# Kernel tuning notes

Hardware: AMD Instinct MI355X
Metric: run time of the kernel (lower is better)

The kernel has to match this reference:

```python
import jax, jax.numpy as jnp
import numpy as np

N_USERS = 100_000
N_ITEMS = 100_000
D = 64
B = 16_384
L_U = 50   # items per user history
N_F = 32   # friends per user
L_I = 50   # users per item history


def setup_inputs() -> dict:
    key = jax.random.key(0)
    ks = jax.random.split(key, 22)
    s = 0.1  # xavier-ish scale for D=64
    return {
        "user_ids": jax.random.randint(ks[0], (B,), 0, N_USERS),
        "item_ids": jax.random.randint(ks[1], (B,), 0, N_ITEMS),
        "user_hist_items": jax.random.randint(ks[2], (B, L_U), 0, N_ITEMS),
        "user_hist_ratings": jax.random.uniform(ks[3], (B, L_U), jnp.float32, 1.0, 5.0),
        "user_friends": jax.random.randint(ks[4], (B, N_F), 0, N_USERS),
        "item_hist_users": jax.random.randint(ks[5], (B, L_I), 0, N_USERS),
        "item_hist_ratings": jax.random.uniform(ks[6], (B, L_I), jnp.float32, 1.0, 5.0),
        "embed_user": jax.random.normal(ks[7], (N_USERS, D), jnp.float32) * s,
        "embed_item": jax.random.normal(ks[8], (N_ITEMS, D), jnp.float32) * s,
        "W1": jax.random.normal(ks[9], (D, D), jnp.float32) * s,
        "W2": jax.random.normal(ks[10], (D, D), jnp.float32) * s,
        "W3": jax.random.normal(ks[11], (D, 1), jnp.float32) * s,
        "W4": jax.random.normal(ks[12], (D, D), jnp.float32) * s,
        "W5": jax.random.normal(ks[13], (D, D), jnp.float32) * s,
        "W6": jax.random.normal(ks[14], (D, 1), jnp.float32) * s,
        "W7": jax.random.normal(ks[15], (D, D), jnp.float32) * s,
        "W8": jax.random.normal(ks[16], (D, D), jnp.float32) * s,
        "W9": jax.random.normal(ks[17], (D, 1), jnp.float32) * s,
        "fc1_w": jax.random.normal(ks[18], (2 * D, D), jnp.float32) * s,
        "fc1_b": jnp.zeros((D,), jnp.float32),
        "fc2_w": jax.random.normal(ks[19], (D, 1), jnp.float32) * s,
        "fc2_b": jnp.zeros((1,), jnp.float32),
    }


def _attention(q_emb, neigh, Wq, Wk, Wa, ratings=None):
    # q_emb: [B, D]; neigh: [B, L, D]; ratings: [B, L] or None
    a = q_emb @ Wq  # [B, D]
    a = a[:, None, :] + neigh @ Wk  # [B, L, D]
    if ratings is not None:
        a = a + ratings[..., None] * neigh
    w = jax.nn.softmax((a @ Wa)[..., 0], axis=1)  # [B, L]
    return jnp.einsum("bl,bld->bd", w, neigh)


def reference(user_ids, item_ids, user_hist_items, user_hist_ratings,
              user_friends, item_hist_users, item_hist_ratings,
              embed_user, embed_item,
              W1, W2, W3, W4, W5, W6, W7, W8, W9,
              fc1_w, fc1_b, fc2_w, fc2_b):
    user_emb = embed_user[user_ids]          # [B, D]
    item_emb = embed_item[item_ids]          # [B, D]

    # user <- rated items attention (W1, W2, W3)
    hist_item_embs = embed_item[user_hist_items]        # [B, L_U, D]
    user_items_emb = _attention(user_emb, hist_item_embs, W1, W2, W3,
                                user_hist_ratings)

    # user <- friends attention (W4, W5, W6)
    friend_embs = embed_user[user_friends]               # [B, N_F, D]
    user_social_emb = _attention(user_emb, friend_embs, W4, W5, W6)

    user_emb_final = user_emb + user_items_emb + user_social_emb

    # item <- interacting users attention (W7, W8, W9)
    hist_user_embs = embed_user[item_hist_users]         # [B, L_I, D]
    item_users_emb = _attention(item_emb, hist_user_embs, W7, W8, W9,
                                item_hist_ratings)
    item_emb_final = item_emb + item_users_emb

    concat = jnp.concatenate([user_emb_final, item_emb_final], axis=1)  # [B, 2D]
    h = jax.nn.relu(concat @ fc1_w + fc1_b)
    out = (h @ fc2_w + fc2_b)[:, 0]  # [B]
    return out
```

## Files before the change

kernel.cpp:

```cpp
#include <hip/hip_runtime.h>
#include <math.h>

#define B_TOTAL 16384
#define D 64
#define L_U 50
#define N_F 32
#define L_I 50

#define WAVE_FL 512

__global__ void graphrec_setup(const float* __restrict__ W2, const float* __restrict__ W3,
                               const float* __restrict__ W5, const float* __restrict__ W6,
                               const float* __restrict__ W8, const float* __restrict__ W9,
                               float* __restrict__ u) {
    int t = threadIdx.x;
    int w = t >> 6;
    int d = t & 63;
    const float* Wm;
    const float* Wv;
    int off;
    switch (w) {
        case 0: Wm = W2; Wv = W3; off = 64;  break;
        case 1: Wm = W5; Wv = W6; off = 192; break;
        default: Wm = W8; Wv = W9; off = 320; break;
    }
    float s = 0.f;
    #pragma unroll
    for (int j = 0; j < D; ++j) s = fmaf(Wm[d * D + j], Wv[j], s);
    u[off + d] = s;
}

__device__ __forceinline__ float wred_sum(float x) {
    float t;
    #define STEP_ADD(ctrl, rmask)                                                        \
        t = __int_as_float(__builtin_amdgcn_update_dpp(0, __float_as_int(x),             \
                                                       ctrl, rmask, 0xf, false));        \
        x = x + t;
    STEP_ADD(0x111, 0xf)
    STEP_ADD(0x112, 0xf)
    STEP_ADD(0x114, 0xf)
    STEP_ADD(0x118, 0xf)
    STEP_ADD(0x142, 0xa)
    STEP_ADD(0x143, 0xc)
    #undef STEP_ADD
    return __int_as_float(__builtin_amdgcn_readlane(__float_as_int(x), 63));
}

__device__ __forceinline__ float segred8(float x) {
    float t;
    t = __int_as_float(__builtin_amdgcn_update_dpp(0, __float_as_int(x), 0x111, 0xf, 0xf, false));
    x = x + t;
    t = __int_as_float(__builtin_amdgcn_update_dpp(0, __float_as_int(x), 0x112, 0xf, 0xf, false));
    x = x + t;
    t = __int_as_float(__builtin_amdgcn_update_dpp(0, __float_as_int(x), 0x114, 0xf, 0xf, false));
    x = x + t;
    return x;
}

__device__ __forceinline__ float dot8(float4 n0, float4 n1, float4 u0, float4 u1) {
    return fmaf(n0.x, u0.x, fmaf(n0.y, u0.y, fmaf(n0.z, u0.z, fmaf(n0.w, u0.w,
           fmaf(n1.x, u1.x, fmaf(n1.y, u1.y, fmaf(n1.z, u1.z, n1.w * u1.w)))))));
}

template <int L, int NG, bool HAS_R>
__device__ __forceinline__ float attn_online(const float* __restrict__ u2,
                                             const float* __restrict__ wa, float rv,
                                             int lane, int sub, int cc, int co,
                                             const float* __restrict__ table, int idxreg,
                                             float* __restrict__ part) {
    const float4 uu0 = ((const float4*)u2)[2 * cc];
    const float4 uu1 = ((const float4*)u2)[2 * cc + 1];
    float4 ww0 = {0.f, 0.f, 0.f, 0.f}, ww1 = {0.f, 0.f, 0.f, 0.f};
    if (HAS_R) {
        ww0 = ((const float4*)wa)[2 * cc];
        ww1 = ((const float4*)wa)[2 * cc + 1];
    }

    float4 st0[2], st1[2];
    float srr[2] = {0.f, 0.f};
    #pragma unroll
    for (int p = 0; p < 2; ++p) {
        const int slot = 8 * p + sub;
        const int rid = __builtin_amdgcn_ds_bpermute(slot << 2, idxreg);
        if (HAS_R)
            srr[p] = __int_as_float(
                __builtin_amdgcn_ds_bpermute(slot << 2, __float_as_int(rv)));
        const float* pp = table + (unsigned)((rid << 6) + co);
        st0[p] = ((const float4*)pp)[0];
        st1[p] = ((const float4*)pp)[1];
    }

    float sum = 0.f;
    float4 a0 = {0.f, 0.f, 0.f, 0.f}, a1 = {0.f, 0.f, 0.f, 0.f};
    #pragma unroll
    for (int g = 0; g < NG; ++g) {
        const int pi = g & 1;
        const float4 n0 = st0[pi];
        const float4 n1 = st1[pi];
        const float rrow = srr[pi];
        if (g + 2 < NG) {
            const int slot2 = 8 * (g + 2) + sub;
            const int sl2 = (slot2 > L - 1) ? (L - 1) : slot2;
            const int rid2 = __builtin_amdgcn_ds_bpermute(sl2 << 2, idxreg);
            if (HAS_R)
                srr[pi] = __int_as_float(
                    __builtin_amdgcn_ds_bpermute(sl2 << 2, __float_as_int(rv)));
            const float* pp2 = table + (unsigned)((rid2 << 6) + co);
            st0[pi] = ((const float4*)pp2)[0];
            st1[pi] = ((const float4*)pp2)[1];
        }
        float4 c0, c1;
        if (HAS_R) {
            c0.x = fmaf(rrow, ww0.x, uu0.x); c0.y = fmaf(rrow, ww0.y, uu0.y);
            c0.z = fmaf(rrow, ww0.z, uu0.z); c0.w = fmaf(rrow, ww0.w, uu0.w);
            c1.x = fmaf(rrow, ww1.x, uu1.x); c1.y = fmaf(rrow, ww1.y, uu1.y);
            c1.z = fmaf(rrow, ww1.z, uu1.z); c1.w = fmaf(rrow, ww1.w, uu1.w);
        } else {
            c0 = uu0; c1 = uu1;
        }
        const float pd = segred8(dot8(n0, n1, c0, c1));
        float e = __expf(__int_as_float(
            __builtin_amdgcn_ds_swizzle(__float_as_int(pd), 0xF8)));
        if (8 * g + sub >= L) e = 0.f;
        sum += e;
        a0.x = fmaf(e, n0.x, a0.x); a0.y = fmaf(e, n0.y, a0.y);
        a0.z = fmaf(e, n0.z, a0.z); a0.w = fmaf(e, n0.w, a0.w);
        a1.x = fmaf(e, n1.x, a1.x); a1.y = fmaf(e, n1.y, a1.y);
        a1.z = fmaf(e, n1.z, a1.z); a1.w = fmaf(e, n1.w, a1.w);
    }

    const float S = wred_sum((cc == 7) ? sum : 0.f);

    const int s4 = lane & 4;
    const int pw = lane << 3;
    *(float4*)(part + pw + s4)       = a0;
    *(float4*)(part + pw + (4 ^ s4)) = a1;
    const int rb = (lane & 56) + ((lane & 7) ^ ((lane >> 3) & 4));
    float acc = 0.f;
    #pragma unroll
    for (int s2 = 0; s2 < 8; ++s2) acc += part[rb + 64 * s2];
    return acc * (1.0f / S);
}

__global__ __launch_bounds__(256) void graphrec_fwd(
        const int* __restrict__ user_ids, const int* __restrict__ item_ids,
        const int* __restrict__ uh_items, const float* __restrict__ uh_rat,
        const int* __restrict__ ufriends,
        const int* __restrict__ ih_users, const float* __restrict__ ih_rat,
        const float* __restrict__ eu, const float* __restrict__ ei,
        const float* __restrict__ W3, const float* __restrict__ W6,
        const float* __restrict__ W9,
        const float* __restrict__ fc1w, const float* __restrict__ fc1b,
        const float* __restrict__ fc2w, const float* __restrict__ fc2b,
        const float* __restrict__ u, float* __restrict__ out) {
    __shared__ __align__(16) float smem[4 * WAVE_FL];
    const int lane = threadIdx.x & 63;
    const int wv = threadIdx.x >> 6;
    const int b = blockIdx.x * 4 + wv;
    float* part = smem + wv * WAVE_FL;
    const int sub = lane >> 3;
    const int cc  = lane & 7;
    const int co  = cc << 3;

    int idxA = 0, idxB = 0, idxC = 0;
    float rA = 0.f, rC = 0.f;
    if (lane < L_U) {
        idxA = uh_items[b * L_U + lane];
        rA   = uh_rat[b * L_U + lane];
        idxC = ih_users[b * L_I + lane];
        rC   = ih_rat[b * L_I + lane];
    }
    if (lane < N_F) idxB = ufriends[b * N_F + lane];

    const int uid = user_ids[b];
    const int iid = item_ids[b];
    const float qu = eu[(size_t)uid * D + lane];
    const float qi = ei[(size_t)iid * D + lane];

    const float accA = attn_online<L_U, 7, true >(u + 64, W3, rA,
                                                  lane, sub, cc, co, ei, idxA, part);
    const float accB = attn_online<N_F, 4, false>(u + 192, W6, 0.f,
                                                  lane, sub, cc, co, eu, idxB, part);
    const float accC = attn_online<L_I, 7, true >(u + 320, W9, rC,
                                                  lane, sub, cc, co, eu, idxC, part);

    const float uf  = qu + accA + accB;
    const float itf = qi + accC;

    float h0 = fc1b[lane], h1 = 0.f, h2 = 0.f, h3 = 0.f;
    #pragma unroll
    for (int k = 0; k < D; k += 4) {
        h0 = fmaf(__int_as_float(__builtin_amdgcn_readlane(__float_as_int(uf), k + 0)),
                  fc1w[(k + 0) * D + lane], h0);
        h1 = fmaf(__int_as_float(__builtin_amdgcn_readlane(__float_as_int(uf), k + 1)),
                  fc1w[(k + 1) * D + lane], h1);
        h2 = fmaf(__int_as_float(__builtin_amdgcn_readlane(__float_as_int(uf), k + 2)),
                  fc1w[(k + 2) * D + lane], h2);
        h3 = fmaf(__int_as_float(__builtin_amdgcn_readlane(__float_as_int(uf), k + 3)),
                  fc1w[(k + 3) * D + lane], h3);
    }
    #pragma unroll
    for (int k = 0; k < D; k += 4) {
        h0 = fmaf(__int_as_float(__builtin_amdgcn_readlane(__float_as_int(itf), k + 0)),
                  fc1w[(D + k + 0) * D + lane], h0);
        h1 = fmaf(__int_as_float(__builtin_amdgcn_readlane(__float_as_int(itf), k + 1)),
                  fc1w[(D + k + 1) * D + lane], h1);
        h2 = fmaf(__int_as_float(__builtin_amdgcn_readlane(__float_as_int(itf), k + 2)),
                  fc1w[(D + k + 2) * D + lane], h2);
        h3 = fmaf(__int_as_float(__builtin_amdgcn_readlane(__float_as_int(itf), k + 3)),
                  fc1w[(D + k + 3) * D + lane], h3);
    }
    const float h = fmaxf((h0 + h1) + (h2 + h3), 0.f);
    const float o = wred_sum(h * fc2w[lane]);
    if (lane == 0) out[b] = o + fc2b[0];
}

extern "C" void kernel_launch(void* const* d_in, const int* in_sizes, int n_in,
                              void* d_out, int out_size, void* d_ws, size_t ws_size,
                              hipStream_t stream) {
    const int*   user_ids = (const int*)d_in[0];
    const int*   item_ids = (const int*)d_in[1];
    const int*   uh_items = (const int*)d_in[2];
    const float* uh_rat   = (const float*)d_in[3];
    const int*   ufriends = (const int*)d_in[4];
    const int*   ih_users = (const int*)d_in[5];
    const float* ih_rat   = (const float*)d_in[6];
    const float* eu       = (const float*)d_in[7];
    const float* ei       = (const float*)d_in[8];
    const float* W3 = (const float*)d_in[11];
    const float* W6 = (const float*)d_in[14];
    const float* W9 = (const float*)d_in[17];
    const float* W2 = (const float*)d_in[10];
    const float* W5 = (const float*)d_in[13];
    const float* W8 = (const float*)d_in[16];
    const float* fc1w = (const float*)d_in[18];
    const float* fc1b = (const float*)d_in[19];
    const float* fc2w = (const float*)d_in[20];
    const float* fc2b = (const float*)d_in[21];
    float* out = (float*)d_out;
    float* u   = (float*)d_ws;

    graphrec_setup<<<1, 192, 0, stream>>>(W2, W3, W5, W6, W8, W9, u);
    graphrec_fwd<<<B_TOTAL / 4, 256, 0, stream>>>(
        user_ids, item_ids, uh_items, uh_rat, ufriends, ih_users, ih_rat,
        eu, ei, W3, W6, W9, fc1w, fc1b, fc2w, fc2b, u, out);
}
```

Measured before the change: 200.8 us.

## Stream neighbor rows via async global-to-LDS ring with deep cross-phase prefetch

Replaces the register double-buffered gathers with direct global_load_lds copies into a 7-slot per-wave LDS ring. One continuous stream of 34 groups spans all three attention phases, kept 6 groups ahead with explicit vmcnt waits, so later phases' gathers overlap earlier compute. Each lane now covers 4 columns with 4 rows per group instead of 8 columns and 8 rows, and the coefficient vectors are staged once in shared memory. In exchange it needs more LDS per block, hand-counted waitcnt values that must match the issue order, and more loop iterations with longer reductions.

```diff
diff --git a/kernel.cpp b/kernel.cpp
--- a/kernel.cpp
+++ b/kernel.cpp
@@ -7,7 +7,21 @@
 #define N_F 32
 #define L_I 50
 
-#define WAVE_FL 512
+#define NG_A 13
+#define NG_B 8
+#define NG_C 13
+#define NSTREAM 34
+#define NSLOT 7
+#define SLOT_FL 256
+#define RING_FL (NSLOT * SLOT_FL)
+#define FOLD_FL 256
+#define WAVE_FL (RING_FL + FOLD_FL)
+#define COEF_FL 320
+
+#define WAITV(n) asm volatile("s_waitcnt vmcnt(" #n ")" ::: "memory")
+
+typedef unsigned int u32_g __attribute__((address_space(1)));
+typedef unsigned int u32_l __attribute__((address_space(3)));
 
 __global__ void graphrec_setup(const float* __restrict__ W2, const float* __restrict__ W3,
                                const float* __restrict__ W5, const float* __restrict__ W6,
@@ -46,7 +60,7 @@
     return __int_as_float(__builtin_amdgcn_readlane(__float_as_int(x), 63));
 }
 
-__device__ __forceinline__ float segred8(float x) {
+__device__ __forceinline__ float segred16(float x) {
     float t;
     t = __int_as_float(__builtin_amdgcn_update_dpp(0, __float_as_int(x), 0x111, 0xf, 0xf, false));
     x = x + t;
@@ -54,91 +68,77 @@
     x = x + t;
     t = __int_as_float(__builtin_amdgcn_update_dpp(0, __float_as_int(x), 0x114, 0xf, 0xf, false));
     x = x + t;
+    t = __int_as_float(__builtin_amdgcn_update_dpp(0, __float_as_int(x), 0x118, 0xf, 0xf, false));
+    x = x + t;
     return x;
 }
 
-__device__ __forceinline__ float dot8(float4 n0, float4 n1, float4 u0, float4 u1) {
-    return fmaf(n0.x, u0.x, fmaf(n0.y, u0.y, fmaf(n0.z, u0.z, fmaf(n0.w, u0.w,
-           fmaf(n1.x, u1.x, fmaf(n1.y, u1.y, fmaf(n1.z, u1.z, n1.w * u1.w)))))));
-}
-
-template <int L, int NG, bool HAS_R>
-__device__ __forceinline__ float attn_online(const float* __restrict__ u2,
-                                             const float* __restrict__ wa, float rv,
-                                             int lane, int sub, int cc, int co,
-                                             const float* __restrict__ table, int idxreg,
-                                             float* __restrict__ part) {
-    const float4 uu0 = ((const float4*)u2)[2 * cc];
-    const float4 uu1 = ((const float4*)u2)[2 * cc + 1];
-    float4 ww0 = {0.f, 0.f, 0.f, 0.f}, ww1 = {0.f, 0.f, 0.f, 0.f};
-    if (HAS_R) {
-        ww0 = ((const float4*)wa)[2 * cc];
-        ww1 = ((const float4*)wa)[2 * cc + 1];
-    }
-
-    float4 st0[2], st1[2];
-    float srr[2] = {0.f, 0.f};
-    #pragma unroll
-    for (int p = 0; p < 2; ++p) {
-        const int slot = 8 * p + sub;
-        const int rid = __builtin_amdgcn_ds_bpermute(slot << 2, idxreg);
-        if (HAS_R)
-            srr[p] = __int_as_float(
-                __builtin_amdgcn_ds_bpermute(slot << 2, __float_as_int(rv)));
-        const float* pp = table + (unsigned)((rid << 6) + co);
-        st0[p] = ((const float4*)pp)[0];
-        st1[p] = ((const float4*)pp)[1];
-    }
+__device__ __forceinline__ void issue_group(int j, int sub, int cl,
+                                            const float* __restrict__ eu,
+                                            const float* __restrict__ ei,
+                                            int idxA, int idxB, int idxC,
+                                            float* ring) {
+    const float* table;
+    int idx, slot, L;
+    if (j < NG_A)               { table = ei; idx = idxA; slot = 4 * j + sub;            L = L_U; }
+    else if (j < NG_A + NG_B)   { table = eu; idx = idxB; slot = 4 * (j - NG_A) + sub;   L = N_F; }
+    else                        { table = eu; idx = idxC; slot = 4 * (j - NG_A - NG_B) + sub; L = L_I; }
+    if (slot > L - 1) slot = L - 1;
+    const int rid = __builtin_amdgcn_ds_bpermute(slot << 2, idx);
+    const float* g = table + (unsigned)((rid << 6) + (cl << 2));
+    float* dst = ring + (j % NSLOT) * SLOT_FL;
+    __builtin_amdgcn_global_load_lds((const u32_g*)g, (u32_l*)dst, 16, 0, 0);
+}
+
+template <int JBASE, int NG, int L, bool HAS_R>
+__device__ __forceinline__ float phase_run(const float* __restrict__ cf_u2,
+                                           const float* __restrict__ cf_wa,
+                                           float rv, int lane, int sub, int cl,
+                                           const float* __restrict__ eu,
+                                           const float* __restrict__ ei,
+                                           int idxA, int idxB, int idxC,
+                                           float* ring, float* fold) {
+    const float4 uu = *(const float4*)(cf_u2 + (cl << 2));
+    float4 ww = {0.f, 0.f, 0.f, 0.f};
+    if (HAS_R) ww = *(const float4*)(cf_wa + (cl << 2));
 
     float sum = 0.f;
-    float4 a0 = {0.f, 0.f, 0.f, 0.f}, a1 = {0.f, 0.f, 0.f, 0.f};
+    float4 a = {0.f, 0.f, 0.f, 0.f};
     #pragma unroll
     for (int g = 0; g < NG; ++g) {
-        const int pi = g & 1;
-        const float4 n0 = st0[pi];
-        const float4 n1 = st1[pi];
-        const float rrow = srr[pi];
-        if (g + 2 < NG) {
-            const int slot2 = 8 * (g + 2) + sub;
-            const int sl2 = (slot2 > L - 1) ? (L - 1) : slot2;
-            const int rid2 = __builtin_amdgcn_ds_bpermute(sl2 << 2, idxreg);
-            if (HAS_R)
-                srr[pi] = __int_as_float(
-                    __builtin_amdgcn_ds_bpermute(sl2 << 2, __float_as_int(rv)));
-            const float* pp2 = table + (unsigned)((rid2 << 6) + co);
-            st0[pi] = ((const float4*)pp2)[0];
-            st1[pi] = ((const float4*)pp2)[1];
+        const int J = JBASE + g;
+        if (J <= 28)      WAITV(5);
+        else if (J == 29) WAITV(4);
+        else if (J == 30) WAITV(3);
+        else if (J == 31) WAITV(2);
+        else if (J == 32) WAITV(1);
+        else              WAITV(0);
+        if (J + 6 < NSTREAM)
+            issue_group(J + 6, sub, cl, eu, ei, idxA, idxB, idxC, ring);
+        const float4 n = *(const float4*)(ring + (J % NSLOT) * SLOT_FL + (lane << 2));
+        float4 c = uu;
+        if (HAS_R) {
+            const int slot = 4 * g + sub;
+            const int sl = (slot > L - 1) ? (L - 1) : slot;
+            const float rrow = __int_as_float(
+                __builtin_amdgcn_ds_bpermute(sl << 2, __float_as_int(rv)));
+            c.x = fmaf(rrow, ww.x, uu.x); c.y = fmaf(rrow, ww.y, uu.y);
+            c.z = fmaf(rrow, ww.z, uu.z); c.w = fmaf(rrow, ww.w, uu.w);
         }
-        float4 c0, c1;
-        if (HAS_R) {
-            c0.x = fmaf(rrow, ww0.x, uu0.x); c0.y = fmaf(rrow, ww0.y, uu0.y);
-            c0.z = fmaf(rrow, ww0.z, uu0.z); c0.w = fmaf(rrow, ww0.w, uu0.w);
-            c1.x = fmaf(rrow, ww1.x, uu1.x); c1.y = fmaf(rrow, ww1.y, uu1.y);
-            c1.z = fmaf(rrow, ww1.z, uu1.z); c1.w = fmaf(rrow, ww1.w, uu1.w);
-        } else {
-            c0 = uu0; c1 = uu1;
-        }
-        const float pd = segred8(dot8(n0, n1, c0, c1));
+        float pd = fmaf(n.x, c.x, fmaf(n.y, c.y, fmaf(n.z, c.z, n.w * c.w)));
+        pd = segred16(pd);
         float e = __expf(__int_as_float(
-            __builtin_amdgcn_ds_swizzle(__float_as_int(pd), 0xF8)));
-        if (8 * g + sub >= L) e = 0.f;
+            __builtin_amdgcn_ds_swizzle(__float_as_int(pd), 0x1FF)));
+        if (4 * g + sub >= L) e = 0.f;
         sum += e;
-        a0.x = fmaf(e, n0.x, a0.x); a0.y = fmaf(e, n0.y, a0.y);
-        a0.z = fmaf(e, n0.z, a0.z); a0.w = fmaf(e, n0.w, a0.w);
-        a1.x = fmaf(e, n1.x, a1.x); a1.y = fmaf(e, n1.y, a1.y);
-        a1.z = fmaf(e, n1.z, a1.z); a1.w = fmaf(e, n1.w, a1.w);
-    }
-
-    const float S = wred_sum((cc == 7) ? sum : 0.f);
-
-    const int s4 = lane & 4;
-    const int pw = lane << 3;
-    *(float4*)(part + pw + s4)       = a0;
-    *(float4*)(part + pw + (4 ^ s4)) = a1;
-    const int rb = (lane & 56) + ((lane & 7) ^ ((lane >> 3) & 4));
-    float acc = 0.f;
-    #pragma unroll
-    for (int s2 = 0; s2 < 8; ++s2) acc += part[rb + 64 * s2];
+        a.x = fmaf(e, n.x, a.x); a.y = fmaf(e, n.y, a.y);
+        a.z = fmaf(e, n.z, a.z); a.w = fmaf(e, n.w, a.w);
+    }
+
+    const float S = wred_sum(((lane & 15) == 15) ? sum : 0.f);
+
+    *(float4*)(fold + (lane << 2)) = a;
+    const float acc = fold[lane] + fold[64 + lane] + fold[128 + lane] + fold[192 + lane];
     return acc * (1.0f / S);
 }
 
@@ -153,14 +153,28 @@
         const float* __restrict__ fc1w, const float* __restrict__ fc1b,
         const float* __restrict__ fc2w, const float* __restrict__ fc2b,
         const float* __restrict__ u, float* __restrict__ out) {
-    __shared__ __align__(16) float smem[4 * WAVE_FL];
+    __shared__ __align__(16) float smem[4 * WAVE_FL + COEF_FL];
     const int lane = threadIdx.x & 63;
     const int wv = threadIdx.x >> 6;
     const int b = blockIdx.x * 4 + wv;
-    float* part = smem + wv * WAVE_FL;
-    const int sub = lane >> 3;
-    const int cc  = lane & 7;
-    const int co  = cc << 3;
+    float* ring = smem + wv * WAVE_FL;
+    float* fold = ring + RING_FL;
+    float* cf   = smem + 4 * WAVE_FL;
+    const int sub = lane >> 4;
+    const int cl  = lane & 15;
+
+    for (int k = threadIdx.x; k < COEF_FL; k += 256) {
+        const int v = k >> 6, d = k & 63;
+        float val;
+        switch (v) {
+            case 0: val = u[64 + d];  break;
+            case 1: val = W3[d];      break;
+            case 2: val = u[192 + d]; break;
+            case 3: val = u[320 + d]; break;
+            default: val = W9[d];     break;
+        }
+        cf[k] = val;
+    }
 
     int idxA = 0, idxB = 0, idxC = 0;
     float rA = 0.f, rC = 0.f;
@@ -177,12 +191,18 @@
     const float qu = eu[(size_t)uid * D + lane];
     const float qi = ei[(size_t)iid * D + lane];
 
-    const float accA = attn_online<L_U, 7, true >(u + 64, W3, rA,
-                                                  lane, sub, cc, co, ei, idxA, part);
-    const float accB = attn_online<N_F, 4, false>(u + 192, W6, 0.f,
-                                                  lane, sub, cc, co, eu, idxB, part);
-    const float accC = attn_online<L_I, 7, true >(u + 320, W9, rC,
-                                                  lane, sub, cc, co, eu, idxC, part);
+    __syncthreads();
+
+    #pragma unroll
+    for (int j = 0; j < 6; ++j)
+        issue_group(j, sub, cl, eu, ei, idxA, idxB, idxC, ring);
+
+    const float accA = phase_run<0,          NG_A, L_U, true >(cf,       cf + 64, rA,
+                            lane, sub, cl, eu, ei, idxA, idxB, idxC, ring, fold);
+    const float accB = phase_run<NG_A,       NG_B, N_F, false>(cf + 128, cf,      0.f,
+                            lane, sub, cl, eu, ei, idxA, idxB, idxC, ring, fold);
+    const float accC = phase_run<NG_A + NG_B, NG_C, L_I, true >(cf + 192, cf + 256, rC,
+                            lane, sub, cl, eu, ei, idxA, idxB, idxC, ring, fold);
 
     const float uf  = qu + accA + accB;
     const float itf = qi + accC;
@@ -227,12 +247,12 @@
     const float* ih_rat   = (const float*)d_in[6];
     const float* eu       = (const float*)d_in[7];
     const float* ei       = (const float*)d_in[8];
+    const float* W2 = (const float*)d_in[10];
     const float* W3 = (const float*)d_in[11];
+    const float* W5 = (const float*)d_in[13];
     const float* W6 = (const float*)d_in[14];
+    const float* W8 = (const float*)d_in[16];
     const float* W9 = (const float*)d_in[17];
-    const float* W2 = (const float*)d_in[10];
-    const float* W5 = (const float*)d_in[13];
-    const float* W8 = (const float*)d_in[16];
     const float* fc1w = (const float*)d_in[18];
     const float* fc1b = (const float*)d_in[19];
     const float* fc2w = (const float*)d_in[20];
```

Result: no change. 198.8 us (-1.0%).

## Gather neighbor embeddings from fp16 copies of the tables converted each call

Applied to the files above, without the earlier changes.

Adds a kernel that converts both full embedding tables (100k x 64 each) to fp16 in the workspace on every call. The attention gathers then read half-width rows and widen them to fp32. The explicit two-deep register prefetch pipeline is replaced with a plain per-group load under a bounds guard. This aims to halve gather traffic, but converting the tables costs about 51 MB read and 25 MB written per call, which likely outweighs the savings on roughly 2.15M random row gathers. It also lowers precision of the neighbor embeddings.

```diff
diff --git a/kernel.cpp b/kernel.cpp
--- a/kernel.cpp
+++ b/kernel.cpp
@@ -1,4 +1,5 @@
 #include <hip/hip_runtime.h>
+#include <hip/hip_fp16.h>
 #include <math.h>
 
 #define B_TOTAL 16384
@@ -6,6 +7,8 @@
 #define L_U 50
 #define N_F 32
 #define L_I 50
+#define N_ROWS 100000
+#define TAB_ELEMS (N_ROWS * D)
 
 #define WAVE_FL 512
 
@@ -30,6 +33,23 @@
     u[off + d] = s;
 }
 
+__global__ void convert_tables(const float* __restrict__ eu, const float* __restrict__ ei,
+                               __half* __restrict__ euh, __half* __restrict__ eih) {
+    const int n4 = TAB_ELEMS / 4;
+    for (int i = blockIdx.x * 256 + threadIdx.x; i < 2 * n4; i += 2048 * 256) {
+        const bool first = (i < n4);
+        const int j = first ? i : i - n4;
+        const float4 v = first ? ((const float4*)eu)[j] : ((const float4*)ei)[j];
+        const __half2 h0 = __float22half2_rn(make_float2(v.x, v.y));
+        const __half2 h1 = __float22half2_rn(make_float2(v.z, v.w));
+        uint2 pk;
+        pk.x = *(const unsigned int*)&h0;
+        pk.y = *(const unsigned int*)&h1;
+        if (first) ((uint2*)euh)[j] = pk;
+        else       ((uint2*)eih)[j] = pk;
+    }
+}
+
 __device__ __forceinline__ float wred_sum(float x) {
     float t;
     #define STEP_ADD(ctrl, rmask)                                                        \
@@ -62,11 +82,11 @@
            fmaf(n1.x, u1.x, fmaf(n1.y, u1.y, fmaf(n1.z, u1.z, n1.w * u1.w)))))));
 }
 
-template <int L, int NG, bool HAS_R>
+template <int L, int NG, bool HAS_R, typename T>
 __device__ __forceinline__ float attn_online(const float* __restrict__ u2,
                                              const float* __restrict__ wa, float rv,
-                                             int lane, int sub, int cc, int co,
-                                             const float* __restrict__ table, int idxreg,
+                                             int lane, int sub, int cc,
+                                             const T* __restrict__ table, int idxreg,
                                              float* __restrict__ part) {
     const float4 uu0 = ((const float4*)u2)[2 * cc];
     const float4 uu1 = ((const float4*)u2)[2 * cc + 1];
@@ -76,57 +96,48 @@
         ww1 = ((const float4*)wa)[2 * cc + 1];
     }
 
-    float4 st0[2], st1[2];
-    float srr[2] = {0.f, 0.f};
-    #pragma unroll
-    for (int p = 0; p < 2; ++p) {
-        const int slot = 8 * p + sub;
-        const int rid = __builtin_amdgcn_ds_bpermute(slot << 2, idxreg);
-        if (HAS_R)
-            srr[p] = __int_as_float(
-                __builtin_amdgcn_ds_bpermute(slot << 2, __float_as_int(rv)));
-        const float* pp = table + (unsigned)((rid << 6) + co);
-        st0[p] = ((const float4*)pp)[0];
-        st1[p] = ((const float4*)pp)[1];
-    }
-
     float sum = 0.f;
     float4 a0 = {0.f, 0.f, 0.f, 0.f}, a1 = {0.f, 0.f, 0.f, 0.f};
     #pragma unroll
     for (int g = 0; g < NG; ++g) {
-        const int pi = g & 1;
-        const float4 n0 = st0[pi];
-        const float4 n1 = st1[pi];
-        const float rrow = srr[pi];
-        if (g + 2 < NG) {
-            const int slot2 = 8 * (g + 2) + sub;
-            const int sl2 = (slot2 > L - 1) ? (L - 1) : slot2;
-            const int rid2 = __builtin_amdgcn_ds_bpermute(sl2 << 2, idxreg);
-            if (HAS_R)
-                srr[pi] = __int_as_float(
-                    __builtin_amdgcn_ds_bpermute(sl2 << 2, __float_as_int(rv)));
-            const float* pp2 = table + (unsigned)((rid2 << 6) + co);
-            st0[pi] = ((const float4*)pp2)[0];
-            st1[pi] = ((const float4*)pp2)[1];
+        const int slot = 8 * g + sub;
+        const int rowid = __builtin_amdgcn_ds_bpermute(slot << 2, idxreg);
+        float rrow = 0.f;
+        if (HAS_R)
+            rrow = __int_as_float(
+                __builtin_amdgcn_ds_bpermute(slot << 2, __float_as_int(rv)));
+        if (slot < L) {
+            float4 n0, n1;
+            const T* p = table + (unsigned)((rowid << 6) + (cc << 3));
+            if constexpr (sizeof(T) == 2) {
+                const int4 raw = *(const int4*)p;
+                float2 f;
+                f = __half22float2(*(const __half2*)&raw.x); n0.x = f.x; n0.y = f.y;
+                f = __half22float2(*(const __half2*)&raw.y); n0.z = f.x; n0.w = f.y;
+                f = __half22float2(*(const __half2*)&raw.z); n1.x = f.x; n1.y = f.y;
+                f = __half22float2(*(const __half2*)&raw.w); n1.z = f.x; n1.w = f.y;
+            } else {
+                n0 = ((const float4*)p)[0];
+                n1 = ((const float4*)p)[1];
+            }
+            float4 c0, c1;
+            if (HAS_R) {
+                c0.x = fmaf(rrow, ww0.x, uu0.x); c0.y = fmaf(rrow, ww0.y, uu0.y);
+                c0.z = fmaf(rrow, ww0.z, uu0.z); c0.w = fmaf(rrow, ww0.w, uu0.w);
+                c1.x = fmaf(rrow, ww1.x, uu1.x); c1.y = fmaf(rrow, ww1.y, uu1.y);
+                c1.z = fmaf(rrow, ww1.z, uu1.z); c1.w = fmaf(rrow, ww1.w, uu1.w);
+            } else {
+                c0 = uu0; c1 = uu1;
+            }
+            const float pd = segred8(dot8(n0, n1, c0, c1));
+            const float e = __expf(__int_as_float(
+                __builtin_amdgcn_ds_swizzle(__float_as_int(pd), 0xF8)));
+            sum += e;
+            a0.x = fmaf(e, n0.x, a0.x); a0.y = fmaf(e, n0.y, a0.y);
+            a0.z = fmaf(e, n0.z, a0.z); a0.w = fmaf(e, n0.w, a0.w);
+            a1.x = fmaf(e, n1.x, a1.x); a1.y = fmaf(e, n1.y, a1.y);
+            a1.z = fmaf(e, n1.z, a1.z); a1.w = fmaf(e, n1.w, a1.w);
         }
-        float4 c0, c1;
-        if (HAS_R) {
-            c0.x = fmaf(rrow, ww0.x, uu0.x); c0.y = fmaf(rrow, ww0.y, uu0.y);
-            c0.z = fmaf(rrow, ww0.z, uu0.z); c0.w = fmaf(rrow, ww0.w, uu0.w);
-            c1.x = fmaf(rrow, ww1.x, uu1.x); c1.y = fmaf(rrow, ww1.y, uu1.y);
-            c1.z = fmaf(rrow, ww1.z, uu1.z); c1.w = fmaf(rrow, ww1.w, uu1.w);
-        } else {
-            c0 = uu0; c1 = uu1;
-        }
-        const float pd = segred8(dot8(n0, n1, c0, c1));
-        float e = __expf(__int_as_float(
-            __builtin_amdgcn_ds_swizzle(__float_as_int(pd), 0xF8)));
-        if (8 * g + sub >= L) e = 0.f;
-        sum += e;
-        a0.x = fmaf(e, n0.x, a0.x); a0.y = fmaf(e, n0.y, a0.y);
-        a0.z = fmaf(e, n0.z, a0.z); a0.w = fmaf(e, n0.w, a0.w);
-        a1.x = fmaf(e, n1.x, a1.x); a1.y = fmaf(e, n1.y, a1.y);
-        a1.z = fmaf(e, n1.z, a1.z); a1.w = fmaf(e, n1.w, a1.w);
     }
 
     const float S = wred_sum((cc == 7) ? sum : 0.f);
@@ -142,14 +153,15 @@
     return acc * (1.0f / S);
 }
 
+template <typename T>
 __global__ __launch_bounds__(256) void graphrec_fwd(
         const int* __restrict__ user_ids, const int* __restrict__ item_ids,
         const int* __restrict__ uh_items, const float* __restrict__ uh_rat,
         const int* __restrict__ ufriends,
         const int* __restrict__ ih_users, const float* __restrict__ ih_rat,
         const float* __restrict__ eu, const float* __restrict__ ei,
-        const float* __restrict__ W3, const float* __restrict__ W6,
-        const float* __restrict__ W9,
+        const T* __restrict__ tabU, const T* __restrict__ tabI,
+        const float* __restrict__ W3, const float* __restrict__ W9,
         const float* __restrict__ fc1w, const float* __restrict__ fc1b,
         const float* __restrict__ fc2w, const float* __restrict__ fc2b,
         const float* __restrict__ u, float* __restrict__ out) {
@@ -160,7 +172,6 @@
     float* part = smem + wv * WAVE_FL;
     const int sub = lane >> 3;
     const int cc  = lane & 7;
-    const int co  = cc << 3;
 
     int idxA = 0, idxB = 0, idxC = 0;
     float rA = 0.f, rC = 0.f;
@@ -177,12 +188,12 @@
     const float qu = eu[(size_t)uid * D + lane];
     const float qi = ei[(size_t)iid * D + lane];
 
-    const float accA = attn_online<L_U, 7, true >(u + 64, W3, rA,
-                                                  lane, sub, cc, co, ei, idxA, part);
-    const float accB = attn_online<N_F, 4, false>(u + 192, W6, 0.f,
-                                                  lane, sub, cc, co, eu, idxB, part);
-    const float accC = attn_online<L_I, 7, true >(u + 320, W9, rC,
-                                                  lane, sub, cc, co, eu, idxC, part);
+    const float accA = attn_online<L_U, 7, true, T>(u + 64, W3, rA,
+                                                    lane, sub, cc, tabI, idxA, part);
+    const float accB = attn_online<N_F, 4, false, T>(u + 192, W3, 0.f,
+                                                     lane, sub, cc, tabU, idxB, part);
+    const float accC = attn_online<L_I, 7, true, T>(u + 320, W9, rC,
+                                                    lane, sub, cc, tabU, idxC, part);
 
     const float uf  = qu + accA + accB;
     const float itf = qi + accC;
@@ -227,12 +238,12 @@
     const float* ih_rat   = (const float*)d_in[6];
     const float* eu       = (const float*)d_in[7];
     const float* ei       = (const float*)d_in[8];
+    const float* W2 = (const float*)d_in[10];
     const float* W3 = (const float*)d_in[11];
+    const float* W5 = (const float*)d_in[13];
     const float* W6 = (const float*)d_in[14];
+    const float* W8 = (const float*)d_in[16];
     const float* W9 = (const float*)d_in[17];
-    const float* W2 = (const float*)d_in[10];
-    const float* W5 = (const float*)d_in[13];
-    const float* W8 = (const float*)d_in[16];
     const float* fc1w = (const float*)d_in[18];
     const float* fc1b = (const float*)d_in[19];
     const float* fc2w = (const float*)d_in[20];
@@ -241,7 +252,18 @@
     float* u   = (float*)d_ws;
 
     graphrec_setup<<<1, 192, 0, stream>>>(W2, W3, W5, W6, W8, W9, u);
-    graphrec_fwd<<<B_TOTAL / 4, 256, 0, stream>>>(
-        user_ids, item_ids, uh_items, uh_rat, ufriends, ih_users, ih_rat,
-        eu, ei, W3, W6, W9, fc1w, fc1b, fc2w, fc2b, u, out);
-}
+
+    const size_t need = 2048 + 2 * (size_t)TAB_ELEMS * sizeof(__half);
+    if (ws_size >= need) {
+        __half* euh = (__half*)((char*)d_ws + 2048);
+        __half* eih = euh + TAB_ELEMS;
+        convert_tables<<<2048, 256, 0, stream>>>(eu, ei, euh, eih);
+        graphrec_fwd<__half><<<B_TOTAL / 4, 256, 0, stream>>>(
+            user_ids, item_ids, uh_items, uh_rat, ufriends, ih_users, ih_rat,
+            eu, ei, euh, eih, W3, W9, fc1w, fc1b, fc2w, fc2b, u, out);
+    } else {
+        graphrec_fwd<float><<<B_TOTAL / 4, 256, 0, stream>>>(
+            user_ids, item_ids, uh_items, uh_rat, ufriends, ih_users, ih_rat,
+            eu, ei, eu, ei, W3, W9, fc1w, fc1b, fc2w, fc2b, u, out);
+    }
+}
```

Measured after the change: 182.6 us. -9.1%, faster.
